# Optimization experiments

Measured on AMD Instinct MI355X. Metric: run time of the kernel, lower is better.

## Reference

```python
import jax, jax.numpy as jnp
import numpy as np

IN_DIMS = 512
TOKEN_DIM = 512
NUM_HEADS = 1
D = TOKEN_DIM * NUM_HEADS
SCALE = TOKEN_DIM ** (-0.5)
EPS = 1e-12  # torch F.normalize default


def _l2norm(v, axis):
    n = jnp.sqrt(jnp.sum(v * v, axis=axis, keepdims=True))
    return v / jnp.maximum(n, EPS)


def setup_inputs() -> dict:
    key = jax.random.key(0)
    ks = jax.random.split(key, 10)
    B, C, H, W = 64, IN_DIMS, 28, 28
    s_in = IN_DIMS ** -0.5
    s_d = D ** -0.5
    return {
        "x": jax.random.normal(ks[0], (B, C, H, W), jnp.float32),
        "Wq": jax.random.normal(ks[1], (IN_DIMS, D), jnp.float32) * s_in,
        "bq": jax.random.normal(ks[2], (D,), jnp.float32) * 0.01,
        "Wk": jax.random.normal(ks[3], (IN_DIMS, D), jnp.float32) * s_in,
        "bk": jax.random.normal(ks[4], (D,), jnp.float32) * 0.01,
        "w_g": jax.random.normal(ks[5], (D, 1), jnp.float32),
        "Wp": jax.random.normal(ks[6], (D, D), jnp.float32) * s_d,
        "bp": jax.random.normal(ks[7], (D,), jnp.float32) * 0.01,
        "Wf": jax.random.normal(ks[8], (D, TOKEN_DIM), jnp.float32) * s_d,
        "bf": jax.random.normal(ks[9], (TOKEN_DIM,), jnp.float32) * 0.01,
    }


def reference(x, Wq, bq, Wk, bk, w_g, Wp, bp, Wf, bf):
    B, C, H, W = x.shape
    t = x.reshape(B, C, H * W).transpose(0, 2, 1)          # [B, N, C]
    query = _l2norm(t @ Wq + bq, axis=-1)                  # [B, N, D]
    k = _l2norm(t @ Wk + bk, axis=-1)                      # [B, N, D]
    attn = _l2norm((query @ w_g) * SCALE, axis=1)          # [B, N, 1], normalized over tokens
    ctx = jnp.sum(attn * query, axis=1, keepdims=True)     # [B, 1, D] global context
    out = (ctx * k) @ Wp + bp + query                      # [B, N, D]
    out = out @ Wf + bf                                    # [B, N, TOKEN_DIM]
    return out.transpose(0, 2, 1).reshape(B, -1, H, W)
```

## Files before the change

kernel.cpp:

```cpp
#include <hip/hip_runtime.h>

#define EPSN 1e-12f
#define SCALE_F 0.044194173824159216f

typedef __bf16 bf16x8 __attribute__((ext_vector_type(8)));
typedef __bf16 bf16x4 __attribute__((ext_vector_type(4)));
typedef float  f32x4  __attribute__((ext_vector_type(4)));

__device__ __forceinline__ void gld16(const void* src, void* dst) {
  __builtin_amdgcn_global_load_lds(
      (const __attribute__((address_space(1))) unsigned int*)src,
      (__attribute__((address_space(3))) unsigned int*)dst, 16, 0, 0);
}

__global__ __launch_bounds__(256) void k_prep_t(const float* __restrict__ Wq,
                                                const float* __restrict__ Wk,
                                                __bf16* __restrict__ WqT,
                                                __bf16* __restrict__ WkT) {
  __shared__ float Tq[32][33], Tk[32][33];
  const int c0 = blockIdx.x * 32, d0 = blockIdx.y * 32;
  const int dx = threadIdx.x, cy = threadIdx.y;
  #pragma unroll
  for (int p = 0; p < 4; ++p) {
    int c = cy + p * 8;
    Tq[c][dx] = Wq[(size_t)(c0 + c) * 512 + d0 + dx];
    Tk[c][dx] = Wk[(size_t)(c0 + c) * 512 + d0 + dx];
  }
  __syncthreads();
  #pragma unroll
  for (int p = 0; p < 4; ++p) {
    int d = cy + p * 8;
    WqT[(size_t)(d0 + d) * 512 + c0 + dx] = (__bf16)Tq[dx][d];
    WkT[(size_t)(d0 + d) * 512 + c0 + dx] = (__bf16)Tk[dx][d];
  }
}

__global__ __launch_bounds__(512) void k_prep_w(const float* __restrict__ Wp,
                                                const float* __restrict__ Wf,
                                                const float* __restrict__ bp,
                                                const float* __restrict__ bfv,
                                                __bf16* __restrict__ WcT,
                                                float* __restrict__ bpf) {
  int kk = blockIdx.x;
  int d  = threadIdx.x;
  float a0 = 0.f, a1 = 0.f, a2 = 0.f, a3 = 0.f;
  for (int c = 0; c < 512; c += 4) {
    a0 = fmaf(Wp[kk * 512 + c],     Wf[(size_t)c * 512 + d],         a0);
    a1 = fmaf(Wp[kk * 512 + c + 1], Wf[(size_t)(c + 1) * 512 + d],   a1);
    a2 = fmaf(Wp[kk * 512 + c + 2], Wf[(size_t)(c + 2) * 512 + d],   a2);
    a3 = fmaf(Wp[kk * 512 + c + 3], Wf[(size_t)(c + 3) * 512 + d],   a3);
  }
  WcT[(size_t)d * 1024 + kk]       = (__bf16)((a0 + a1) + (a2 + a3));
  WcT[(size_t)d * 1024 + 512 + kk] = (__bf16)Wf[(size_t)kk * 512 + d];
  if (kk == 0) {
    float b0 = 0.f, b1 = 0.f;
    for (int c = 0; c < 512; c += 2) {
      b0 = fmaf(bp[c],     Wf[(size_t)c * 512 + d],       b0);
      b1 = fmaf(bp[c + 1], Wf[(size_t)(c + 1) * 512 + d], b1);
    }
    bpf[d] = b0 + b1 + bfv[d];
  }
}

__global__ __launch_bounds__(512, 4) void k_qk(const float* __restrict__ x,
                                               const __bf16* __restrict__ WqT,
                                               const __bf16* __restrict__ WkT,
                                               const float* __restrict__ bq,
                                               const float* __restrict__ bk,
                                               const float* __restrict__ wg,
                                               __bf16* __restrict__ Qn,
                                               __bf16* __restrict__ Kn,
                                               float* __restrict__ pctx,
                                               float* __restrict__ pgsq) {
  __shared__ __align__(1024) unsigned char stg[36864];
  __shared__ float red[8][64], redG[8][64], invv[64], gs[64];
  const int t = threadIdx.x, lane = t & 63, w = t >> 6;
  const int li = lane & 15, lq = lane >> 4;
  const int n0 = blockIdx.x * 64, b = blockIdx.y, isK = blockIdx.z;
  const __bf16* Wt  = isK ? WkT : WqT;
  const float* bias = isK ? bk : bq;
  __bf16* dst       = isK ? Kn : Qn;

  const int stok = t & 63, scp = (t >> 6) * 4;
  const bool nv = (n0 + stok < 784);
  const float* xp = x + ((size_t)b * 512 + scp) * 784 + n0 + stok;
  const __bf16* wsrc = Wt + (size_t)((w * 4) * 16 + (lane >> 2)) * 512 + (lane & 3) * 8;

  f32x4 acc[4][4] = {};

  for (int ks = 0; ks < 16; ++ks) {
    const int k0 = ks * 32;
    #pragma unroll
    for (int i = 0; i < 4; ++i) {
      int r = w * 4 + i;
      gld16(wsrc + (size_t)i * 16 * 512 + k0, (void*)(stg + 4096 + r * 1024));
    }
    {
      float v0 = nv ? xp[(size_t)(k0 + 0) * 784] : 0.f;
      float v1 = nv ? xp[(size_t)(k0 + 1) * 784] : 0.f;
      float v2 = nv ? xp[(size_t)(k0 + 2) * 784] : 0.f;
      float v3 = nv ? xp[(size_t)(k0 + 3) * 784] : 0.f;
      bf16x4 v; v[0] = (__bf16)v0; v[1] = (__bf16)v1; v[2] = (__bf16)v2; v[3] = (__bf16)v3;
      *(bf16x4*)(stg + stok * 64 + scp * 2) = v;
    }
    __syncthreads();
    bf16x8 af[4];
    #pragma unroll
    for (int rb = 0; rb < 4; ++rb)
      af[rb] = *(const bf16x8*)(stg + (rb * 16 + li) * 64 + lq * 16);
    #pragma unroll
    for (int cb = 0; cb < 4; ++cb) {
      bf16x8 bf = *(const bf16x8*)(stg + 4096 + (w * 64 + cb * 16 + li) * 64 + lq * 16);
      #pragma unroll
      for (int rb = 0; rb < 4; ++rb)
        acc[rb][cb] = __builtin_amdgcn_mfma_f32_16x16x32_bf16(af[rb], bf, acc[rb][cb], 0, 0, 0);
    }
    __syncthreads();
  }

  float bv[4], wv[4];
  #pragma unroll
  for (int cb = 0; cb < 4; ++cb) {
    int col = w * 64 + cb * 16 + li;
    bv[cb] = bias[col];
    wv[cb] = isK ? 0.f : wg[col];
  }
  #pragma unroll
  for (int rb = 0; rb < 4; ++rb)
    #pragma unroll
    for (int cb = 0; cb < 4; ++cb)
      #pragma unroll
      for (int j = 0; j < 4; ++j)
        acc[rb][cb][j] += bv[cb];
  #pragma unroll
  for (int rb = 0; rb < 4; ++rb)
    #pragma unroll
    for (int j = 0; j < 4; ++j) {
      float ss = 0.f, sg = 0.f;
      #pragma unroll
      for (int cb = 0; cb < 4; ++cb) {
        float v = acc[rb][cb][j];
        ss = fmaf(v, v, ss); sg = fmaf(v, wv[cb], sg);
      }
      ss += __shfl_xor(ss, 1); ss += __shfl_xor(ss, 2); ss += __shfl_xor(ss, 4); ss += __shfl_xor(ss, 8);
      sg += __shfl_xor(sg, 1); sg += __shfl_xor(sg, 2); sg += __shfl_xor(sg, 4); sg += __shfl_xor(sg, 8);
      if (li == 0) {
        int row = rb * 16 + lq * 4 + j;
        red[w][row] = ss; redG[w][row] = sg;
      }
    }
  __syncthreads();
  if (t < 64) {
    float ss = 0.f, sg = 0.f;
    #pragma unroll
    for (int wv2 = 0; wv2 < 8; ++wv2) { ss += red[wv2][t]; sg += redG[wv2][t]; }
    float iv = 1.f / fmaxf(sqrtf(ss), EPSN);
    invv[t] = iv;
    if (!isK) {
      float gv = (n0 + t < 784) ? sg * iv : 0.f;
      gs[t] = gv;
      float pg = gv * gv;
      pg += __shfl_xor(pg, 1);  pg += __shfl_xor(pg, 2);  pg += __shfl_xor(pg, 4);
      pg += __shfl_xor(pg, 8);  pg += __shfl_xor(pg, 16); pg += __shfl_xor(pg, 32);
      if (t == 0) pgsq[b * 13 + blockIdx.x] = pg;
    }
  }
  __syncthreads();
  float pc[4] = {0.f, 0.f, 0.f, 0.f};
  #pragma unroll
  for (int rb = 0; rb < 4; ++rb)
    #pragma unroll
    for (int j = 0; j < 4; ++j) {
      int row = rb * 16 + lq * 4 + j;
      if (n0 + row < 784) {
        float iv = invv[row];
        float gr = isK ? 0.f : gs[row];
        size_t base = ((size_t)b * 784 + n0 + row) * 512 + w * 64 + li;
        #pragma unroll
        for (int cb = 0; cb < 4; ++cb) {
          float qv = acc[rb][cb][j] * iv;
          dst[base + cb * 16] = (__bf16)qv;
          pc[cb] = fmaf(gr, qv, pc[cb]);
        }
      }
    }
  if (!isK) {
    #pragma unroll
    for (int cb = 0; cb < 4; ++cb) {
      pc[cb] += __shfl_xor(pc[cb], 16);
      pc[cb] += __shfl_xor(pc[cb], 32);
    }
    if (lq == 0) {
      #pragma unroll
      for (int cb = 0; cb < 4; ++cb)
        pctx[((size_t)b * 13 + blockIdx.x) * 512 + w * 64 + cb * 16 + li] = pc[cb];
    }
  }
}

__global__ __launch_bounds__(512) void k_ctx2(const float* __restrict__ pctx,
                                              const float* __restrict__ pgsq,
                                              float* __restrict__ ctx) {
  const int b = blockIdx.x, t = threadIdx.x;
  float tot = 0.f;
  #pragma unroll
  for (int i = 0; i < 13; ++i) tot += pgsq[b * 13 + i];
  float alpha = SCALE_F / fmaxf(sqrtf(tot) * SCALE_F, EPSN);
  float s = 0.f;
  #pragma unroll
  for (int i = 0; i < 13; ++i) s += pctx[((size_t)b * 13 + i) * 512 + t];
  ctx[(size_t)b * 512 + t] = alpha * s;
}

__global__ __launch_bounds__(512) void k_kc(__bf16* __restrict__ Kn,
                                            const float* __restrict__ ctx) {
  const int b = blockIdx.y;
  const int chunk = blockIdx.x * 512 + threadIdx.x;
  const int row = chunk >> 6;
  const int c8 = (chunk & 63) * 8;
  __bf16* p = Kn + ((size_t)b * 784 + row) * 512 + c8;
  const float* cp = ctx + b * 512 + c8;
  bf16x8 v = *(const bf16x8*)p;
  #pragma unroll
  for (int j = 0; j < 8; ++j) v[j] = (__bf16)((float)v[j] * cp[j]);
  *(bf16x8*)p = v;
}

__global__ __launch_bounds__(512, 4) void k_out(const __bf16* __restrict__ Qn,
                                                const __bf16* __restrict__ Kc,
                                                const __bf16* __restrict__ WcT,
                                                const float* __restrict__ bpf,
                                                float* __restrict__ out) {
  __shared__ __align__(1024) unsigned char stg[36864];
  const int t = threadIdx.x, lane = t & 63, w = t >> 6;
  const int li = lane & 15, lq = lane >> 4;
  const int n0 = blockIdx.x * 64, b = blockIdx.y;
  size_t grow = (size_t)b * 784 + n0 + (lane >> 2);
  f32x4 acc[4][4] = {};

  for (int ks = 0; ks < 32; ++ks) {
    const int k0 = ks * 32;
    const __bf16* Arow = (ks < 16) ? Kc : Qn;
    const int kA = (ks < 16) ? k0 : k0 - 512;
    #pragma unroll
    for (int i = 0; i < 5; ++i) {
      int r = w + i * 8;
      if (r < 36) {
        void* dstl = (void*)(stg + r * 1024);
        if (r < 4) {
          size_t gr = grow + r * 16;
          if (gr > 50175) gr = 50175;
          gld16(Arow + gr * 512 + kA + (lane & 3) * 8, dstl);
        } else {
          int dr = (r - 4) * 16 + (lane >> 2);
          gld16(WcT + (size_t)dr * 1024 + k0 + (lane & 3) * 8, dstl);
        }
      }
    }
    __syncthreads();
    bf16x8 af[4];
    #pragma unroll
    for (int rb = 0; rb < 4; ++rb)
      af[rb] = *(const bf16x8*)(stg + (rb * 16 + li) * 64 + lq * 16);
    #pragma unroll
    for (int cb = 0; cb < 4; ++cb) {
      bf16x8 bf = *(const bf16x8*)(stg + 4096 + (w * 64 + cb * 16 + li) * 64 + lq * 16);
      #pragma unroll
      for (int rb = 0; rb < 4; ++rb)
        acc[rb][cb] = __builtin_amdgcn_mfma_f32_16x16x32_bf16(af[rb], bf, acc[rb][cb], 0, 0, 0);
    }
    __syncthreads();
  }

  float bv[4];
  #pragma unroll
  for (int cb = 0; cb < 4; ++cb) bv[cb] = bpf[w * 64 + cb * 16 + li];
  #pragma unroll
  for (int rb = 0; rb < 4; ++rb) {
    int nrow = n0 + rb * 16 + lq * 4;
    if (nrow < 784) {
      #pragma unroll
      for (int cb = 0; cb < 4; ++cb) {
        f32x4 v;
        #pragma unroll
        for (int j = 0; j < 4; ++j) v[j] = acc[rb][cb][j] + bv[cb];
        *(f32x4*)&out[((size_t)b * 512 + w * 64 + cb * 16 + li) * 784 + nrow] = v;
      }
    }
  }
}

extern "C" void kernel_launch(void* const* d_in, const int* in_sizes, int n_in,
                              void* d_out, int out_size, void* d_ws, size_t ws_size,
                              hipStream_t stream) {
  const float* x   = (const float*)d_in[0];
  const float* Wq  = (const float*)d_in[1];
  const float* bq  = (const float*)d_in[2];
  const float* Wk  = (const float*)d_in[3];
  const float* bk  = (const float*)d_in[4];
  const float* wg  = (const float*)d_in[5];
  const float* Wp  = (const float*)d_in[6];
  const float* bp  = (const float*)d_in[7];
  const float* Wf  = (const float*)d_in[8];
  const float* bfv = (const float*)d_in[9];
  float* out = (float*)d_out;
  char* ws = (char*)d_ws;

  const size_t SZQN = (size_t)64 * 784 * 512 * 2;
  __bf16* Qn   = (__bf16*)(ws);
  __bf16* Kn   = (__bf16*)(ws + SZQN);
  __bf16* WqT  = (__bf16*)(ws + 2 * SZQN);
  __bf16* WkT  = (__bf16*)(ws + 2 * SZQN + 524288);
  __bf16* WcT  = (__bf16*)(ws + 2 * SZQN + 2 * 524288);
  float*  bpf  = (float*) (ws + 2 * SZQN + 2 * 524288 + 1048576);
  float*  pctx = (float*) (ws + 2 * SZQN + 2 * 524288 + 1048576 + 2048);
  float*  pgsq = (float*) (ws + 2 * SZQN + 2 * 524288 + 1048576 + 2048 + 1703936);
  float*  ctx  = (float*) (ws + 2 * SZQN + 2 * 524288 + 1048576 + 2048 + 1703936 + 4096);

  k_prep_t<<<dim3(16, 16),    dim3(32, 8), 0, stream>>>(Wq, Wk, WqT, WkT);
  k_prep_w<<<dim3(512),       dim3(512),   0, stream>>>(Wp, Wf, bp, bfv, WcT, bpf);
  k_qk    <<<dim3(13, 64, 2), dim3(512),   0, stream>>>(x, WqT, WkT, bq, bk, wg, Qn, Kn, pctx, pgsq);
  k_ctx2  <<<dim3(64),        dim3(512),   0, stream>>>(pctx, pgsq, ctx);
  k_kc    <<<dim3(98, 64),    dim3(512),   0, stream>>>(Kn, ctx);
  k_out   <<<dim3(13, 64),    dim3(512),   0, stream>>>(Qn, Kn, WcT, bpf, out);
}
```

Baseline: 347.2 us.

## Double-buffer LDS staging in QK and output GEMMs with software prefetch

Both GEMM kernels now use two LDS stage buffers so the next K-slice's global loads are issued before computing on the current one, removing one barrier per iteration. In k_qk the x values are prefetched into registers two steps ahead and a custom barrier waits only on older vector loads. The LDS layouts are also rearranged into MFMA-fragment order, and the Q/K blocks are interleaved along blockIdx.x so they share x in cache. Doubled LDS (about 72KB per block) may lower occupancy relative to launch_bounds(512,4).

```diff
diff --git a/kernel.cpp b/kernel.cpp
--- a/kernel.cpp
+++ b/kernel.cpp
@@ -12,6 +12,12 @@
       (const __attribute__((address_space(1))) unsigned int*)src,
       (__attribute__((address_space(3))) unsigned int*)dst, 16, 0, 0);
 }
+
+#define BARRIER_W4() do { \
+  asm volatile("s_waitcnt vmcnt(4) lgkmcnt(0)" ::: "memory"); \
+  __builtin_amdgcn_sched_barrier(0); \
+  __builtin_amdgcn_s_barrier(); \
+  __builtin_amdgcn_sched_barrier(0); } while (0)
 
 __global__ __launch_bounds__(256) void k_prep_t(const float* __restrict__ Wq,
                                                 const float* __restrict__ Wk,
@@ -72,50 +78,76 @@
                                                __bf16* __restrict__ Kn,
                                                float* __restrict__ pctx,
                                                float* __restrict__ pgsq) {
-  __shared__ __align__(1024) unsigned char stg[36864];
+  __shared__ __align__(1024) unsigned char stg[2][36864];
   __shared__ float red[8][64], redG[8][64], invv[64], gs[64];
   const int t = threadIdx.x, lane = t & 63, w = t >> 6;
   const int li = lane & 15, lq = lane >> 4;
-  const int n0 = blockIdx.x * 64, b = blockIdx.y, isK = blockIdx.z;
+  const int isK = blockIdx.x & 1, nx = blockIdx.x >> 1;
+  const int n0 = nx * 64, b = blockIdx.y;
   const __bf16* Wt  = isK ? WkT : WqT;
   const float* bias = isK ? bk : bq;
   __bf16* dst       = isK ? Kn : Qn;
 
-  const int stok = t & 63, scp = (t >> 6) * 4;
-  const bool nv = (n0 + stok < 784);
-  const float* xp = x + ((size_t)b * 512 + scp) * 784 + n0 + stok;
-  const __bf16* wsrc = Wt + (size_t)((w * 4) * 16 + (lane >> 2)) * 512 + (lane & 3) * 8;
-
+  const int ra = w & 3, h = w >> 2;
+  const int tok = ra * 16 + li;
+  int nc = n0 + tok; if (nc > 783) nc = 783;
+  const float* xbase = x + ((size_t)b * 512 + lq * 8 + h * 4) * 784 + nc;
+  const __bf16* wsrc = Wt + (size_t)li * 512 + lq * 8;
+
+  float xA[4], xB[4];
   f32x4 acc[4][4] = {};
 
-  for (int ks = 0; ks < 16; ++ks) {
-    const int k0 = ks * 32;
+  auto loadX = [&](float (&xr)[4], int ks) {
+    if (ks > 15) ks = 15;
+    #pragma unroll
+    for (int j = 0; j < 4; ++j)
+      xr[j] = xbase[(size_t)(ks * 32 + j) * 784];
+  };
+  auto stageB = [&](int buf, int ks) {
     #pragma unroll
     for (int i = 0; i < 4; ++i) {
       int r = w * 4 + i;
-      gld16(wsrc + (size_t)i * 16 * 512 + k0, (void*)(stg + 4096 + r * 1024));
-    }
-    {
-      float v0 = nv ? xp[(size_t)(k0 + 0) * 784] : 0.f;
-      float v1 = nv ? xp[(size_t)(k0 + 1) * 784] : 0.f;
-      float v2 = nv ? xp[(size_t)(k0 + 2) * 784] : 0.f;
-      float v3 = nv ? xp[(size_t)(k0 + 3) * 784] : 0.f;
-      bf16x4 v; v[0] = (__bf16)v0; v[1] = (__bf16)v1; v[2] = (__bf16)v2; v[3] = (__bf16)v3;
-      *(bf16x4*)(stg + stok * 64 + scp * 2) = v;
-    }
-    __syncthreads();
+      gld16(wsrc + (size_t)r * 16 * 512 + ks * 32, stg[buf] + 4096 + r * 1024);
+    }
+  };
+  auto writeA = [&](int buf, const float (&xr)[4]) {
+    bf16x4 v;
+    #pragma unroll
+    for (int j = 0; j < 4; ++j) v[j] = (__bf16)xr[j];
+    *(bf16x4*)(stg[buf] + ra * 1024 + lane * 16 + h * 8) = v;
+  };
+  auto mstep = [&](int buf) {
     bf16x8 af[4];
     #pragma unroll
     for (int rb = 0; rb < 4; ++rb)
-      af[rb] = *(const bf16x8*)(stg + (rb * 16 + li) * 64 + lq * 16);
+      af[rb] = *(const bf16x8*)(stg[buf] + rb * 1024 + lane * 16);
     #pragma unroll
     for (int cb = 0; cb < 4; ++cb) {
-      bf16x8 bf = *(const bf16x8*)(stg + 4096 + (w * 64 + cb * 16 + li) * 64 + lq * 16);
+      bf16x8 bf = *(const bf16x8*)(stg[buf] + 4096 + (w * 4 + cb) * 1024 + lane * 16);
       #pragma unroll
       for (int rb = 0; rb < 4; ++rb)
         acc[rb][cb] = __builtin_amdgcn_mfma_f32_16x16x32_bf16(af[rb], bf, acc[rb][cb], 0, 0, 0);
     }
-    __syncthreads();
+  };
+
+  loadX(xA, 0); loadX(xB, 1);
+  stageB(0, 0); writeA(0, xA);
+  __builtin_amdgcn_sched_barrier(0);
+  loadX(xA, 2);
+  BARRIER_W4();
+
+  #pragma unroll 1
+  for (int k = 0; k < 16; k += 2) {
+    stageB(1, k + 1); writeA(1, xB);
+    __builtin_amdgcn_sched_barrier(0);
+    loadX(xB, k + 3);
+    mstep(0);
+    BARRIER_W4();
+    if (k + 2 < 16) { stageB(0, k + 2); writeA(0, xA); }
+    __builtin_amdgcn_sched_barrier(0);
+    loadX(xA, k + 4);
+    mstep(1);
+    BARRIER_W4();
   }
 
   float bv[4], wv[4];
@@ -162,7 +194,7 @@
       float pg = gv * gv;
       pg += __shfl_xor(pg, 1);  pg += __shfl_xor(pg, 2);  pg += __shfl_xor(pg, 4);
       pg += __shfl_xor(pg, 8);  pg += __shfl_xor(pg, 16); pg += __shfl_xor(pg, 32);
-      if (t == 0) pgsq[b * 13 + blockIdx.x] = pg;
+      if (t == 0) pgsq[b * 13 + nx] = pg;
     }
   }
   __syncthreads();
@@ -193,7 +225,7 @@
     if (lq == 0) {
       #pragma unroll
       for (int cb = 0; cb < 4; ++cb)
-        pctx[((size_t)b * 13 + blockIdx.x) * 512 + w * 64 + cb * 16 + li] = pc[cb];
+        pctx[((size_t)b * 13 + nx) * 512 + w * 64 + cb * 16 + li] = pc[cb];
     }
   }
 }
@@ -231,44 +263,49 @@
                                                 const __bf16* __restrict__ WcT,
                                                 const float* __restrict__ bpf,
                                                 float* __restrict__ out) {
-  __shared__ __align__(1024) unsigned char stg[36864];
+  __shared__ __align__(1024) unsigned char stg[2][36864];
   const int t = threadIdx.x, lane = t & 63, w = t >> 6;
   const int li = lane & 15, lq = lane >> 4;
   const int n0 = blockIdx.x * 64, b = blockIdx.y;
-  size_t grow = (size_t)b * 784 + n0 + (lane >> 2);
   f32x4 acc[4][4] = {};
 
-  for (int ks = 0; ks < 32; ++ks) {
-    const int k0 = ks * 32;
-    const __bf16* Arow = (ks < 16) ? Kc : Qn;
-    const int kA = (ks < 16) ? k0 : k0 - 512;
+  auto stage = [&](int buf, int ks) {
+    const __bf16* Ap = (ks < 16) ? Kc : Qn;
+    const int kA = (ks & 15) * 32;
     #pragma unroll
     for (int i = 0; i < 5; ++i) {
       int r = w + i * 8;
       if (r < 36) {
-        void* dstl = (void*)(stg + r * 1024);
         if (r < 4) {
-          size_t gr = grow + r * 16;
-          if (gr > 50175) gr = 50175;
-          gld16(Arow + gr * 512 + kA + (lane & 3) * 8, dstl);
+          int row = n0 + r * 16 + li; if (row > 783) row = 783;
+          gld16(Ap + ((size_t)b * 784 + row) * 512 + kA + lq * 8, stg[buf] + r * 1024);
         } else {
-          int dr = (r - 4) * 16 + (lane >> 2);
-          gld16(WcT + (size_t)dr * 1024 + k0 + (lane & 3) * 8, dstl);
+          gld16(WcT + (size_t)((r - 4) * 16 + li) * 1024 + ks * 32 + lq * 8,
+                stg[buf] + 4096 + (r - 4) * 1024);
         }
       }
     }
-    __syncthreads();
+  };
+  auto mstep = [&](const unsigned char* s) {
     bf16x8 af[4];
     #pragma unroll
     for (int rb = 0; rb < 4; ++rb)
-      af[rb] = *(const bf16x8*)(stg + (rb * 16 + li) * 64 + lq * 16);
+      af[rb] = *(const bf16x8*)(s + rb * 1024 + lane * 16);
     #pragma unroll
     for (int cb = 0; cb < 4; ++cb) {
-      bf16x8 bf = *(const bf16x8*)(stg + 4096 + (w * 64 + cb * 16 + li) * 64 + lq * 16);
+      bf16x8 bf = *(const bf16x8*)(s + 4096 + (w * 4 + cb) * 1024 + lane * 16);
       #pragma unroll
       for (int rb = 0; rb < 4; ++rb)
         acc[rb][cb] = __builtin_amdgcn_mfma_f32_16x16x32_bf16(af[rb], bf, acc[rb][cb], 0, 0, 0);
     }
+  };
+
+  stage(0, 0);
+  __syncthreads();
+  #pragma unroll 1
+  for (int ks = 0; ks < 32; ++ks) {
+    if (ks + 1 < 32) stage((ks + 1) & 1, ks + 1);
+    mstep(stg[ks & 1]);
     __syncthreads();
   }
 
@@ -317,10 +354,10 @@
   float*  pgsq = (float*) (ws + 2 * SZQN + 2 * 524288 + 1048576 + 2048 + 1703936);
   float*  ctx  = (float*) (ws + 2 * SZQN + 2 * 524288 + 1048576 + 2048 + 1703936 + 4096);
 
-  k_prep_t<<<dim3(16, 16),    dim3(32, 8), 0, stream>>>(Wq, Wk, WqT, WkT);
-  k_prep_w<<<dim3(512),       dim3(512),   0, stream>>>(Wp, Wf, bp, bfv, WcT, bpf);
-  k_qk    <<<dim3(13, 64, 2), dim3(512),   0, stream>>>(x, WqT, WkT, bq, bk, wg, Qn, Kn, pctx, pgsq);
-  k_ctx2  <<<dim3(64),        dim3(512),   0, stream>>>(pctx, pgsq, ctx);
-  k_kc    <<<dim3(98, 64),    dim3(512),   0, stream>>>(Kn, ctx);
-  k_out   <<<dim3(13, 64),    dim3(512),   0, stream>>>(Qn, Kn, WcT, bpf, out);
-}
+  k_prep_t<<<dim3(16, 16), dim3(32, 8), 0, stream>>>(Wq, Wk, WqT, WkT);
+  k_prep_w<<<dim3(512),    dim3(512),   0, stream>>>(Wp, Wf, bp, bfv, WcT, bpf);
+  k_qk    <<<dim3(26, 64), dim3(512),   0, stream>>>(x, WqT, WkT, bq, bk, wg, Qn, Kn, pctx, pgsq);
+  k_ctx2  <<<dim3(64),     dim3(512),   0, stream>>>(pctx, pgsq, ctx);
+  k_kc    <<<dim3(98, 64), dim3(512),   0, stream>>>(Kn, ctx);
+  k_out   <<<dim3(13, 64), dim3(512),   0, stream>>>(Qn, Kn, WcT, bpf, out);
+}
```

Result: slower. 386.2 us (+11.2%).
